# Performance work log

Hardware: AMD Instinct MI355X
Metric: run time of the kernel (lower is better)

Reference implementation:

```python
import jax, jax.numpy as jnp
import numpy as np

N_NODES = 100000
N_EDGES = 1600000


def setup_inputs() -> dict:
    key = jax.random.key(0)
    k1, k2, k3, k4 = jax.random.split(key, 4)
    x = jax.random.normal(k1, (N_NODES, 256), dtype=jnp.float32)
    edge_index = jax.random.randint(k2, (2, N_EDGES), 0, N_NODES, dtype=jnp.int64)
    W1 = jax.random.normal(k3, (256, 128), dtype=jnp.float32) * (1.0 / np.sqrt(256))
    W2 = jax.random.normal(k4, (128, 40), dtype=jnp.float32) * (1.0 / np.sqrt(128))
    return {"x": x, "edge_index": edge_index, "W1": W1, "W2": W2}


def _gcn_conv(x, W, src, dst):
    # GCNConv(normalize=False, add_self_loops=False, bias=False):
    # linear transform then sum-aggregate messages along edges src->dst.
    h = x @ W                                   # [N, d_out]
    msg = h[src]                                # [E, d_out] gather
    return jax.ops.segment_sum(msg, dst, num_segments=N_NODES)  # [N, d_out] scatter-add


def reference(x, edge_index, W1, W2):
    src, dst = edge_index[0], edge_index[1]
    h = jax.nn.relu(_gcn_conv(x, W1, src, dst))
    # dropout is identity in eval mode
    out = _gcn_conv(h, W2, src, dst)
    return out
```

## Files before the change

### kernel.cpp

```cpp
#include <hip/hip_runtime.h>

constexpr int NN = 100000;
constexpr int NE = 1600000;
constexpr int DI = 256, DH = 128, DO = 40;

constexpr int NB = (NN + 255) >> 8;
constexpr int NB_BLK = 128;
constexpr int CHUNK = NE / NB_BLK;
constexpr int M2 = NB * NB_BLK;
constexpr int NBS = (M2 + 1023) / 1024;
constexpr int STAGE_CAP = 6144;
constexpr int WPACK_BLOCKS = 152;
constexpr int GEMM1_BLOCKS = (NN + 63) / 64;

typedef __attribute__((ext_vector_type(8))) __bf16 bf16x8;
typedef __attribute__((ext_vector_type(4))) float f32x4;

__device__ inline float4 bf4_to_f4(ushort4 u) {
    return make_float4(__builtin_bit_cast(float, (unsigned)u.x << 16),
                       __builtin_bit_cast(float, (unsigned)u.y << 16),
                       __builtin_bit_cast(float, (unsigned)u.z << 16),
                       __builtin_bit_cast(float, (unsigned)u.w << 16));
}
__device__ inline unsigned short f2bf(float f) {
    return __builtin_bit_cast(unsigned short, (__bf16)f);
}
__device__ inline bf16x8 bf16x8_zero() {
    bf16x8 r;
    #pragma unroll
    for (int j = 0; j < 8; ++j) r[j] = (__bf16)0.f;
    return r;
}
__device__ inline bf16x8 load_cvt_a(const float* __restrict__ p, bool ok) {
    if (!ok) return bf16x8_zero();
    bf16x8 r;
    const float4 v0 = *(const float4*)p;
    const float4 v1 = *(const float4*)(p + 4);
    r[0] = (__bf16)v0.x; r[1] = (__bf16)v0.y; r[2] = (__bf16)v0.z; r[3] = (__bf16)v0.w;
    r[4] = (__bf16)v1.x; r[5] = (__bf16)v1.y; r[6] = (__bf16)v1.z; r[7] = (__bf16)v1.w;
    return r;
}
__device__ inline void acc4(float4& a, float4 v) {
    a.x += v.x; a.y += v.y; a.z += v.z; a.w += v.w;
}

__global__ __launch_bounds__(256) void wpack_hist_kernel(const float* __restrict__ W1,
                                                         const float* __restrict__ W2,
                                                         const int* __restrict__ dst,
                                                         __bf16* __restrict__ Wf,
                                                         __bf16* __restrict__ Wf2,
                                                         int* __restrict__ hist2d) {
    __shared__ int h[NB];
    if (blockIdx.x < 128) {
        const int i = blockIdx.x * 256 + threadIdx.x;
        const int j = i & 7;
        const int lane = (i >> 3) & 63;
        const int nt = (i >> 9) & 7;
        const int kt = i >> 12;
        const int k = kt * 32 + (lane >> 4) * 8 + j;
        const int n = nt * 16 + (lane & 15);
        Wf[i] = (__bf16)W1[(size_t)k * DH + n];
    } else if (blockIdx.x < WPACK_BLOCKS) {
        const int i = (blockIdx.x - 128) * 256 + threadIdx.x;
        if (i < 6144) {
            const int j = i & 7;
            const int lane = (i >> 3) & 63;
            const int g = i >> 9;
            const int nt = g % 3, ks = g / 3;
            const int k = ks * 32 + (lane >> 4) * 8 + j;
            const int n = nt * 16 + (lane & 15);
            Wf2[i] = (n < DO) ? (__bf16)W2[(size_t)k * DO + n] : (__bf16)0.f;
        }
    } else {
        const int hb = blockIdx.x - WPACK_BLOCKS;
        for (int i = threadIdx.x; i < NB; i += 256) h[i] = 0;
        __syncthreads();
        const int base = hb * CHUNK;
        for (int i = threadIdx.x; i < CHUNK; i += 256)
            atomicAdd(&h[dst[base + i] >> 8], 1);
        __syncthreads();
        for (int i = threadIdx.x; i < NB; i += 256)
            hist2d[i * NB_BLK + hb] = h[i];
    }
}

__global__ __launch_bounds__(256) void gemm1_scan_kernel(const float* __restrict__ x,
                                                         const __bf16* __restrict__ Wf,
                                                         __bf16* __restrict__ h1,
                                                         const int* __restrict__ hist2d,
                                                         int* __restrict__ offs2d) {
    __shared__ int red[256];
    if (blockIdx.x < GEMM1_BLOCKS) {
        const int t = threadIdx.x;
        const int wave = t >> 6, lane = t & 63;
        const int q = lane >> 4, m = lane & 15;
        const int row0 = blockIdx.x * 64 + wave * 16;
        const int r = row0 + m;
        const bool ok = r < NN;
        const float* xp = x + (size_t)r * DI;

        bf16x8 a[8];
        #pragma unroll
        for (int kt = 0; kt < 8; ++kt)
            a[kt] = load_cvt_a(xp + kt * 32 + q * 8, ok);

        f32x4 acc[8];
        #pragma unroll
        for (int nt = 0; nt < 8; ++nt)
            #pragma unroll
            for (int rr = 0; rr < 4; ++rr) acc[nt][rr] = 0.f;

        const bf16x8* wf = (const bf16x8*)Wf;
        #pragma unroll
        for (int kt = 0; kt < 8; ++kt) {
            #pragma unroll
            for (int nt = 0; nt < 8; ++nt) {
                const bf16x8 b = wf[(kt * 8 + nt) * 64 + lane];
                acc[nt] = __builtin_amdgcn_mfma_f32_16x16x32_bf16(a[kt], b, acc[nt], 0, 0, 0);
            }
        }
        #pragma unroll
        for (int reg = 0; reg < 4; ++reg) {
            const int rr = row0 + q * 4 + reg;
            if (rr < NN) {
                __bf16* hp = h1 + (size_t)rr * DH + m;
                #pragma unroll
                for (int nt = 0; nt < 8; ++nt) hp[nt * 16] = (__bf16)acc[nt][reg];
            }
        }
    } else {
        const int b = blockIdx.x - GEMM1_BLOCKS;
        const int t = threadIdx.x;
        int s = 0;
        const int limit = b * 1024;
        for (int i = t * 4; i < limit; i += 1024) {
            const int4 v = *(const int4*)(hist2d + i);
            s += v.x + v.y + v.z + v.w;
        }
        red[t] = s;
        __syncthreads();
        #pragma unroll
        for (int d = 128; d > 0; d >>= 1) {
            if (t < d) red[t] += red[t + d];
            __syncthreads();
        }
        const int base = red[0];
        __syncthreads();
        const int idx = b * 1024 + t * 4;
        int4 v = make_int4(0, 0, 0, 0);
        if (idx < M2) v = *(const int4*)(hist2d + idx);
        const int sl = v.x + v.y + v.z + v.w;
        red[t] = sl;
        __syncthreads();
        for (int d = 1; d < 256; d <<= 1) {
            const int u = (t >= d) ? red[t - d] : 0;
            __syncthreads();
            red[t] += u;
            __syncthreads();
        }
        if (idx < M2) {
            const int e0 = base + red[t] - sl;
            *(int4*)(offs2d + idx) = make_int4(e0, e0 + v.x, e0 + v.x + v.y,
                                               e0 + v.x + v.y + v.z);
        }
    }
}

__global__ __launch_bounds__(256) void bucket_scatter_kernel(const int* __restrict__ src,
                                                             const int* __restrict__ dst,
                                                             const int* __restrict__ offs2d,
                                                             unsigned* __restrict__ epack) {
    __shared__ int cur[NB];
    for (int i = threadIdx.x; i < NB; i += 256)
        cur[i] = offs2d[i * NB_BLK + blockIdx.x];
    __syncthreads();
    const int base = blockIdx.x * CHUNK;
    for (int i = threadIdx.x; i < CHUNK; i += 256) {
        const int d = dst[base + i], s = src[base + i];
        const int p = atomicAdd(&cur[d >> 8], 1);
        epack[p] = (unsigned)s | ((unsigned)(d & 255) << 24);
    }
}

__global__ __launch_bounds__(256) void bucket_sort_kernel(const unsigned* __restrict__ epack,
                                                          const int* __restrict__ offs2d,
                                                          int* __restrict__ off,
                                                          int* __restrict__ esrc) {
    __shared__ int cnt[256];
    __shared__ int incl[256];
    __shared__ int cur[256];
    __shared__ int stage[STAGE_CAP];
    const int b = blockIdx.x;
    const int t = threadIdx.x;
    const int bstart = offs2d[b * NB_BLK];
    const int bend = (b + 1 < NB) ? offs2d[(b + 1) * NB_BLK] : NE;
    const int n = bend - bstart;
    cnt[t] = 0;
    __syncthreads();
    for (int i = t; i < n; i += 256)
        atomicAdd(&cnt[epack[bstart + i] >> 24], 1);
    __syncthreads();
    incl[t] = cnt[t];
    __syncthreads();
    for (int d = 1; d < 256; d <<= 1) {
        const int u = (t >= d) ? incl[t - d] : 0;
        __syncthreads();
        incl[t] += u;
        __syncthreads();
    }
    const int ex = incl[t] - cnt[t];
    const int node = (b << 8) + t;
    if (node <= NN) off[node] = bstart + ex;
    cur[t] = ex;
    __syncthreads();
    const bool staged = (n <= STAGE_CAP);
    for (int i = t; i < n; i += 256) {
        const unsigned pk = epack[bstart + i];
        const int p = atomicAdd(&cur[pk >> 24], 1);
        const int s = (int)(pk & 0xFFFFFFu);
        if (staged) stage[p] = s;
        else esrc[bstart + p] = s;
    }
    __syncthreads();
    if (staged)
        for (int i = t; i < n; i += 256) esrc[bstart + i] = stage[i];
}

__global__ __launch_bounds__(256) void agg1_kernel(const __bf16* __restrict__ h1,
                                                   const int* __restrict__ esrc,
                                                   const int* __restrict__ off,
                                                   __bf16* __restrict__ agg) {
    const int w = (blockIdx.x * 256 + threadIdx.x) >> 6;
    if (w >= NN) return;
    const int lane = threadIdx.x & 63;
    const int half = lane >> 5;
    const int c = (lane & 31) * 4;
    const int b = off[w], e = off[w + 1];
    float4 a0 = make_float4(0.f, 0.f, 0.f, 0.f);
    float4 a1 = a0, a2 = a0, a3 = a0;
    int j = b + half;
    for (; j + 6 < e; j += 8) {
        const int s0 = esrc[j], s1 = esrc[j + 2], s2 = esrc[j + 4], s3 = esrc[j + 6];
        acc4(a0, bf4_to_f4(*(const ushort4*)(h1 + (size_t)s0 * DH + c)));
        acc4(a1, bf4_to_f4(*(const ushort4*)(h1 + (size_t)s1 * DH + c)));
        acc4(a2, bf4_to_f4(*(const ushort4*)(h1 + (size_t)s2 * DH + c)));
        acc4(a3, bf4_to_f4(*(const ushort4*)(h1 + (size_t)s3 * DH + c)));
    }
    for (; j < e; j += 2) {
        const int s = esrc[j];
        acc4(a0, bf4_to_f4(*(const ushort4*)(h1 + (size_t)s * DH + c)));
    }
    float4 acc = make_float4(a0.x + a1.x + a2.x + a3.x,
                             a0.y + a1.y + a2.y + a3.y,
                             a0.z + a1.z + a2.z + a3.z,
                             a0.w + a1.w + a2.w + a3.w);
    acc.x += __shfl_xor(acc.x, 32);
    acc.y += __shfl_xor(acc.y, 32);
    acc.z += __shfl_xor(acc.z, 32);
    acc.w += __shfl_xor(acc.w, 32);
    if (half == 0) {
        ushort4 o;
        o.x = f2bf(fmaxf(acc.x, 0.f));
        o.y = f2bf(fmaxf(acc.y, 0.f));
        o.z = f2bf(fmaxf(acc.z, 0.f));
        o.w = f2bf(fmaxf(acc.w, 0.f));
        *(ushort4*)(agg + (size_t)w * DH + c) = o;
    }
}

__global__ __launch_bounds__(256) void gemm2_kernel(const __bf16* __restrict__ agg,
                                                    const __bf16* __restrict__ Wf2,
                                                    __bf16* __restrict__ h2) {
    const int t = threadIdx.x;
    const int wave = t >> 6, lane = t & 63;
    const int q = lane >> 4, m = lane & 15;
    const int row0 = blockIdx.x * 64 + wave * 16;
    const int r = row0 + m;
    const bool ok = r < NN;
    const __bf16* ap = agg + (size_t)r * DH;

    f32x4 acc[3];
    #pragma unroll
    for (int nt = 0; nt < 3; ++nt)
        #pragma unroll
        for (int rr = 0; rr < 4; ++rr) acc[nt][rr] = 0.f;

    const bf16x8* wf2 = (const bf16x8*)Wf2;
    #pragma unroll
    for (int ks = 0; ks < 4; ++ks) {
        const int k0 = ks * 32 + q * 8;
        const bf16x8 a = ok ? *(const bf16x8*)(ap + k0) : bf16x8_zero();
        #pragma unroll
        for (int nt = 0; nt < 3; ++nt) {
            const bf16x8 b = wf2[(ks * 3 + nt) * 64 + lane];
            acc[nt] = __builtin_amdgcn_mfma_f32_16x16x32_bf16(a, b, acc[nt], 0, 0, 0);
        }
    }
    #pragma unroll
    for (int reg = 0; reg < 4; ++reg) {
        const int rr = row0 + q * 4 + reg;
        if (rr < NN) {
            #pragma unroll
            for (int nt = 0; nt < 3; ++nt) {
                const int cc = nt * 16 + m;
                if (cc < DO) h2[(size_t)rr * DO + cc] = (__bf16)acc[nt][reg];
            }
        }
    }
}

__global__ __launch_bounds__(256) void agg2_kernel(const __bf16* __restrict__ h2,
                                                   const int* __restrict__ esrc,
                                                   const int* __restrict__ off,
                                                   float* __restrict__ out) {
    const int w = (blockIdx.x * 256 + threadIdx.x) >> 6;
    if (w >= NN) return;
    const int lane = threadIdx.x & 63;
    const int sub = lane / 10;
    const int c = (lane % 10) * 4;
    const int b = off[w], e = off[w + 1];
    const int deg = e - b;
    float4 a0 = make_float4(0.f, 0.f, 0.f, 0.f);
    float4 a1 = a0, a2 = a0, a3 = a0;

    for (int base = 0; base < deg; base += 64) {
        const int cnt = min(64, deg - base);
        const int cl = cnt - 1;
        const int idx = (base + lane < deg) ? esrc[b + base + lane] : 0;
        const bool act = sub < 6;
        int kk = 0;
        for (; kk + 24 <= cnt; kk += 24) {
            const int e0 = kk + sub;
            const int s0 = __shfl(idx, min(e0, cl));
            const int s1 = __shfl(idx, min(e0 + 6, cl));
            const int s2 = __shfl(idx, min(e0 + 12, cl));
            const int s3 = __shfl(idx, min(e0 + 18, cl));
            const float4 v0 = bf4_to_f4(*(const ushort4*)(h2 + (size_t)s0 * DO + c));
            const float4 v1 = bf4_to_f4(*(const ushort4*)(h2 + (size_t)s1 * DO + c));
            const float4 v2 = bf4_to_f4(*(const ushort4*)(h2 + (size_t)s2 * DO + c));
            const float4 v3 = bf4_to_f4(*(const ushort4*)(h2 + (size_t)s3 * DO + c));
            if (act) { acc4(a0, v0); acc4(a1, v1); acc4(a2, v2); acc4(a3, v3); }
        }
        for (; kk + 12 <= cnt; kk += 12) {
            const int e0 = kk + sub;
            const int s0 = __shfl(idx, min(e0, cl));
            const int s1 = __shfl(idx, min(e0 + 6, cl));
            const float4 v0 = bf4_to_f4(*(const ushort4*)(h2 + (size_t)s0 * DO + c));
            const float4 v1 = bf4_to_f4(*(const ushort4*)(h2 + (size_t)s1 * DO + c));
            if (act) { acc4(a0, v0); acc4(a1, v1); }
        }
        for (; kk < cnt; kk += 6) {
            const int e0 = kk + sub;
            const int s0 = __shfl(idx, min(e0, cl));
            const float4 v = bf4_to_f4(*(const ushort4*)(h2 + (size_t)s0 * DO + c));
            if (act && e0 < cnt) acc4(a0, v);
        }
    }
    float4 acc = make_float4(a0.x + a1.x + a2.x + a3.x, a0.y + a1.y + a2.y + a3.y,
                             a0.z + a1.z + a2.z + a3.z, a0.w + a1.w + a2.w + a3.w);
    acc.x += __shfl(acc.x, lane + 30);
    acc.y += __shfl(acc.y, lane + 30);
    acc.z += __shfl(acc.z, lane + 30);
    acc.w += __shfl(acc.w, lane + 30);
    const float ax = acc.x + __shfl(acc.x, lane + 10) + __shfl(acc.x, lane + 20);
    const float ay = acc.y + __shfl(acc.y, lane + 10) + __shfl(acc.y, lane + 20);
    const float az = acc.z + __shfl(acc.z, lane + 10) + __shfl(acc.z, lane + 20);
    const float aw = acc.w + __shfl(acc.w, lane + 10) + __shfl(acc.w, lane + 20);
    if (lane < 10) {
        *(float4*)(out + (size_t)w * DO + c) = make_float4(ax, ay, az, aw);
    }
}

extern "C" void kernel_launch(void* const* d_in, const int* in_sizes, int n_in,
                              void* d_out, int out_size, void* d_ws, size_t ws_size,
                              hipStream_t stream) {
    const float* x  = (const float*)d_in[0];
    const int*   ei = (const int*)d_in[1];
    const float* W1 = (const float*)d_in[2];
    const float* W2 = (const float*)d_in[3];
    const int* src = ei;
    const int* dst = ei + NE;

    __bf16* Wf  = (__bf16*)d_ws;
    __bf16* Wf2 = Wf + 32768;
    __bf16* h1  = Wf2 + 6144;
    __bf16* agg = h1 + (size_t)NN * DH;
    __bf16* h2  = h1;
    unsigned* epack = (unsigned*)(agg + (size_t)NN * DH);
    int* esrc   = (int*)(epack + NE);
    int* off    = esrc + NE;
    int* hist2d = off + NN + 1;
    int* offs2d = hist2d + M2;

    float* out = (float*)d_out;

    wpack_hist_kernel<<<WPACK_BLOCKS + NB_BLK, 256, 0, stream>>>(W1, W2, dst, Wf, Wf2, hist2d);
    gemm1_scan_kernel<<<GEMM1_BLOCKS + NBS, 256, 0, stream>>>(x, Wf, h1, hist2d, offs2d);
    bucket_scatter_kernel<<<NB_BLK, 256, 0, stream>>>(src, dst, offs2d, epack);
    bucket_sort_kernel<<<NB, 256, 0, stream>>>(epack, offs2d, off, esrc);
    agg1_kernel<<<(NN * 64 + 255) / 256, 256, 0, stream>>>(h1, esrc, off, agg);
    gemm2_kernel<<<(NN + 63) / 64, 256, 0, stream>>>(agg, Wf2, h2);
    agg2_kernel<<<(NN * 64 + 255) / 256, 256, 0, stream>>>(h2, esrc, off, out);
}
```

Before: 354.8 us.

## Run scan standalone, fuse gemm1 with bucket scatter, unroll agg1 gather by eight

The prefix scan moves into its own small kernel, and the bucket scatter now runs in the same launch as the first GEMM as extra blocks. The scatter's atomic-heavy work can then overlap the compute-bound GEMM instead of running as a separate serial launch. The tiny scan, which used to overlap the GEMM, now runs alone ahead of it. Separately, agg1 gains a 16-edge unrolled loop with eight accumulators to put more gather loads in flight, at the cost of more registers per thread.

```diff
diff --git a/kernel.cpp b/kernel.cpp
--- a/kernel.cpp
+++ b/kernel.cpp
@@ -84,12 +84,53 @@
     }
 }
 
-__global__ __launch_bounds__(256) void gemm1_scan_kernel(const float* __restrict__ x,
-                                                         const __bf16* __restrict__ Wf,
-                                                         __bf16* __restrict__ h1,
-                                                         const int* __restrict__ hist2d,
-                                                         int* __restrict__ offs2d) {
+__global__ __launch_bounds__(256) void scan_kernel(const int* __restrict__ hist2d,
+                                                   int* __restrict__ offs2d) {
     __shared__ int red[256];
+    const int b = blockIdx.x;
+    const int t = threadIdx.x;
+    int s = 0;
+    const int limit = b * 1024;
+    for (int i = t * 4; i < limit; i += 1024) {
+        const int4 v = *(const int4*)(hist2d + i);
+        s += v.x + v.y + v.z + v.w;
+    }
+    red[t] = s;
+    __syncthreads();
+    #pragma unroll
+    for (int d = 128; d > 0; d >>= 1) {
+        if (t < d) red[t] += red[t + d];
+        __syncthreads();
+    }
+    const int base = red[0];
+    __syncthreads();
+    const int idx = b * 1024 + t * 4;
+    int4 v = make_int4(0, 0, 0, 0);
+    if (idx < M2) v = *(const int4*)(hist2d + idx);
+    const int sl = v.x + v.y + v.z + v.w;
+    red[t] = sl;
+    __syncthreads();
+    for (int d = 1; d < 256; d <<= 1) {
+        const int u = (t >= d) ? red[t - d] : 0;
+        __syncthreads();
+        red[t] += u;
+        __syncthreads();
+    }
+    if (idx < M2) {
+        const int e0 = base + red[t] - sl;
+        *(int4*)(offs2d + idx) = make_int4(e0, e0 + v.x, e0 + v.x + v.y,
+                                           e0 + v.x + v.y + v.z);
+    }
+}
+
+__global__ __launch_bounds__(256) void gemm1_scatter_kernel(const float* __restrict__ x,
+                                                            const __bf16* __restrict__ Wf,
+                                                            __bf16* __restrict__ h1,
+                                                            const int* __restrict__ src,
+                                                            const int* __restrict__ dst,
+                                                            const int* __restrict__ offs2d,
+                                                            unsigned* __restrict__ epack) {
+    __shared__ int cur[NB];
     if (blockIdx.x < GEMM1_BLOCKS) {
         const int t = threadIdx.x;
         const int wave = t >> 6, lane = t & 63;
@@ -129,56 +170,16 @@
             }
         }
     } else {
-        const int b = blockIdx.x - GEMM1_BLOCKS;
-        const int t = threadIdx.x;
-        int s = 0;
-        const int limit = b * 1024;
-        for (int i = t * 4; i < limit; i += 1024) {
-            const int4 v = *(const int4*)(hist2d + i);
-            s += v.x + v.y + v.z + v.w;
-        }
-        red[t] = s;
-        __syncthreads();
-        #pragma unroll
-        for (int d = 128; d > 0; d >>= 1) {
-            if (t < d) red[t] += red[t + d];
-            __syncthreads();
-        }
-        const int base = red[0];
-        __syncthreads();
-        const int idx = b * 1024 + t * 4;
-        int4 v = make_int4(0, 0, 0, 0);
-        if (idx < M2) v = *(const int4*)(hist2d + idx);
-        const int sl = v.x + v.y + v.z + v.w;
-        red[t] = sl;
-        __syncthreads();
-        for (int d = 1; d < 256; d <<= 1) {
-            const int u = (t >= d) ? red[t - d] : 0;
-            __syncthreads();
-            red[t] += u;
-            __syncthreads();
-        }
-        if (idx < M2) {
-            const int e0 = base + red[t] - sl;
-            *(int4*)(offs2d + idx) = make_int4(e0, e0 + v.x, e0 + v.x + v.y,
-                                               e0 + v.x + v.y + v.z);
-        }
-    }
-}
-
-__global__ __launch_bounds__(256) void bucket_scatter_kernel(const int* __restrict__ src,
-                                                             const int* __restrict__ dst,
-                                                             const int* __restrict__ offs2d,
-                                                             unsigned* __restrict__ epack) {
-    __shared__ int cur[NB];
-    for (int i = threadIdx.x; i < NB; i += 256)
-        cur[i] = offs2d[i * NB_BLK + blockIdx.x];
-    __syncthreads();
-    const int base = blockIdx.x * CHUNK;
-    for (int i = threadIdx.x; i < CHUNK; i += 256) {
-        const int d = dst[base + i], s = src[base + i];
-        const int p = atomicAdd(&cur[d >> 8], 1);
-        epack[p] = (unsigned)s | ((unsigned)(d & 255) << 24);
+        const int sb = blockIdx.x - GEMM1_BLOCKS;
+        for (int i = threadIdx.x; i < NB; i += 256)
+            cur[i] = offs2d[i * NB_BLK + sb];
+        __syncthreads();
+        const int base = sb * CHUNK;
+        for (int i = threadIdx.x; i < CHUNK; i += 256) {
+            const int d = dst[base + i], s = src[base + i];
+            const int p = atomicAdd(&cur[d >> 8], 1);
+            epack[p] = (unsigned)s | ((unsigned)(d & 255) << 24);
+        }
     }
 }
 
@@ -237,8 +238,20 @@
     const int c = (lane & 31) * 4;
     const int b = off[w], e = off[w + 1];
     float4 a0 = make_float4(0.f, 0.f, 0.f, 0.f);
-    float4 a1 = a0, a2 = a0, a3 = a0;
+    float4 a1 = a0, a2 = a0, a3 = a0, a4 = a0, a5 = a0, a6 = a0, a7 = a0;
     int j = b + half;
+    for (; j + 14 < e; j += 16) {
+        const int s0 = esrc[j],      s1 = esrc[j + 2],  s2 = esrc[j + 4],  s3 = esrc[j + 6];
+        const int s4 = esrc[j + 8],  s5 = esrc[j + 10], s6 = esrc[j + 12], s7 = esrc[j + 14];
+        acc4(a0, bf4_to_f4(*(const ushort4*)(h1 + (size_t)s0 * DH + c)));
+        acc4(a1, bf4_to_f4(*(const ushort4*)(h1 + (size_t)s1 * DH + c)));
+        acc4(a2, bf4_to_f4(*(const ushort4*)(h1 + (size_t)s2 * DH + c)));
+        acc4(a3, bf4_to_f4(*(const ushort4*)(h1 + (size_t)s3 * DH + c)));
+        acc4(a4, bf4_to_f4(*(const ushort4*)(h1 + (size_t)s4 * DH + c)));
+        acc4(a5, bf4_to_f4(*(const ushort4*)(h1 + (size_t)s5 * DH + c)));
+        acc4(a6, bf4_to_f4(*(const ushort4*)(h1 + (size_t)s6 * DH + c)));
+        acc4(a7, bf4_to_f4(*(const ushort4*)(h1 + (size_t)s7 * DH + c)));
+    }
     for (; j + 6 < e; j += 8) {
         const int s0 = esrc[j], s1 = esrc[j + 2], s2 = esrc[j + 4], s3 = esrc[j + 6];
         acc4(a0, bf4_to_f4(*(const ushort4*)(h1 + (size_t)s0 * DH + c)));
@@ -250,10 +263,10 @@
         const int s = esrc[j];
         acc4(a0, bf4_to_f4(*(const ushort4*)(h1 + (size_t)s * DH + c)));
     }
-    float4 acc = make_float4(a0.x + a1.x + a2.x + a3.x,
-                             a0.y + a1.y + a2.y + a3.y,
-                             a0.z + a1.z + a2.z + a3.z,
-                             a0.w + a1.w + a2.w + a3.w);
+    float4 acc = make_float4(a0.x + a1.x + a2.x + a3.x + a4.x + a5.x + a6.x + a7.x,
+                             a0.y + a1.y + a2.y + a3.y + a4.y + a5.y + a6.y + a7.y,
+                             a0.z + a1.z + a2.z + a3.z + a4.z + a5.z + a6.z + a7.z,
+                             a0.w + a1.w + a2.w + a3.w + a4.w + a5.w + a6.w + a7.w);
     acc.x += __shfl_xor(acc.x, 32);
     acc.y += __shfl_xor(acc.y, 32);
     acc.z += __shfl_xor(acc.z, 32);
@@ -395,8 +408,8 @@
     float* out = (float*)d_out;
 
     wpack_hist_kernel<<<WPACK_BLOCKS + NB_BLK, 256, 0, stream>>>(W1, W2, dst, Wf, Wf2, hist2d);
-    gemm1_scan_kernel<<<GEMM1_BLOCKS + NBS, 256, 0, stream>>>(x, Wf, h1, hist2d, offs2d);
-    bucket_scatter_kernel<<<NB_BLK, 256, 0, stream>>>(src, dst, offs2d, epack);
+    scan_kernel<<<NBS, 256, 0, stream>>>(hist2d, offs2d);
+    gemm1_scatter_kernel<<<GEMM1_BLOCKS + NB_BLK, 256, 0, stream>>>(x, Wf, h1, src, dst, offs2d, epack);
     bucket_sort_kernel<<<NB, 256, 0, stream>>>(epack, offs2d, off, esrc);
     agg1_kernel<<<(NN * 64 + 255) / 256, 256, 0, stream>>>(h1, esrc, off, agg);
     gemm2_kernel<<<(NN + 63) / 64, 256, 0, stream>>>(agg, Wf2, h2);
```

After: 373.9 us. 5.4% more time.
